# Performance work log

Measured on AMD Instinct MI355X. Metric: run time of the kernel, lower is better.

The kernel has to match this reference:

```python
import jax, jax.numpy as jnp
import numpy as np

B, D, NCOMP, DCOMP = 4096, 2048, 4, 1024  # out_features = NCOMP * DCOMP = 4096


def setup_inputs() -> dict:
    key = jax.random.key(0)
    ks = jax.random.split(key, 6)
    scale = 0.02
    return {
        "x": jax.random.normal(ks[0], (B, D), jnp.float32),
        "noise": jax.random.normal(ks[1], (B, NCOMP), jnp.float32),
        "Wc": jax.random.normal(ks[2], (NCOMP, D, DCOMP), jnp.float32) * scale,
        "bc": jnp.zeros((NCOMP, DCOMP), jnp.float32),
        "Wg": jax.random.normal(ks[3], (D, NCOMP), jnp.float32) * scale,
        "bg": jnp.zeros((NCOMP,), jnp.float32),
        "Wn": jax.random.normal(ks[4], (D, NCOMP), jnp.float32) * scale,
        "bn": jnp.zeros((NCOMP,), jnp.float32),
    }


def reference(x, noise, Wc, bc, Wg, bg, Wn, bn):
    # gating: H = Wg(x) + randn * softplus(Wnoise(x))
    g = x @ Wg + bg                                   # [B, n]
    sp = jax.nn.softplus(x @ Wn + bn)                 # [B, n]
    H = g + noise * sp                                # [B, n]
    # top-1 index, monotonic hard gate: select all components i <= argmax
    k = jnp.argmax(H, axis=1, keepdims=True)          # [B, 1]
    mask = (jnp.arange(H.shape[1])[None, :] <= k).astype(H.dtype)  # [B, n]
    # straight-through: forward value = mask, grad d G/d H = identity
    G = H + jax.lax.stop_gradient(mask - H)
    # all components computed vectorized; unselected ones are zeroed by G
    comps = jnp.einsum('bd,ndo->bno', x, Wc) + bc     # [B, n, DCOMP]
    mask_sg = jax.lax.stop_gradient(mask)
    # multiply by mask_sg so unselected (padded) channels carry no grad path,
    # matching torch which never computes components beyond k (zero pad).
    E = (comps * G[:, :, None] * mask_sg[:, :, None]).reshape(x.shape[0], -1)  # [B, out_features]
    return (E, G)
```

## Files before the change

kernel.cpp:

```cpp
#include <hip/hip_runtime.h>
#include <hip/hip_bf16.h>
#include <math.h>

constexpr int BROWS = 4096;
constexpr int DDIM  = 2048;
constexpr int NCOMP = 4;
constexpr int DCOMP = 1024;
constexpr int NOUT  = NCOMP * DCOMP;

typedef __attribute__((ext_vector_type(8))) short bf16x8;
typedef __attribute__((ext_vector_type(4))) float f32x4;
typedef __attribute__((ext_vector_type(4))) short s16x4;

__device__ __forceinline__ short f2bf(float f) {
  union { float f; unsigned u; } v; v.f = f;
  unsigned r = v.u + 0x7FFFu + ((v.u >> 16) & 1u);
  return (short)(r >> 16);
}

#define GLOAD_LDS16(gptr, lptr) __builtin_amdgcn_global_load_lds( \
    (const __attribute__((address_space(1))) void*)(gptr),        \
    (__attribute__((address_space(3))) void*)(lptr), 16, 0, 0)

__global__ __launch_bounds__(256) void prep_kernel(
    const float* __restrict__ x, const float* __restrict__ noise,
    const float* __restrict__ Wg, const float* __restrict__ bg,
    const float* __restrict__ Wn, const float* __restrict__ bn,
    const float* __restrict__ Wc,
    float* __restrict__ Gout, short* __restrict__ xb, short* __restrict__ WcT) {
  __shared__ float tile[64][65];
  const int bid = blockIdx.x;
  const int tid = threadIdx.x;

  if (bid < 1024) {
    const int lane = tid & 63;
    const int row  = bid * 4 + (tid >> 6);
    const float* xr = x + (size_t)row * DDIM;
    short* xbr = xb + (size_t)row * DDIM;

    float ag[4] = {0.f, 0.f, 0.f, 0.f};
    float an[4] = {0.f, 0.f, 0.f, 0.f};
#pragma unroll
    for (int i = 0; i < 8; i++) {
      int d = i * 256 + lane * 4;
      float4 v = *reinterpret_cast<const float4*>(xr + d);
      s16x4 s; s.x = f2bf(v.x); s.y = f2bf(v.y); s.z = f2bf(v.z); s.w = f2bf(v.w);
      *reinterpret_cast<s16x4*>(xbr + d) = s;
      float xv[4] = {v.x, v.y, v.z, v.w};
#pragma unroll
      for (int j = 0; j < 4; j++) {
        float4 wg = *reinterpret_cast<const float4*>(Wg + 4 * (d + j));
        float4 wn = *reinterpret_cast<const float4*>(Wn + 4 * (d + j));
        ag[0] += xv[j] * wg.x; ag[1] += xv[j] * wg.y;
        ag[2] += xv[j] * wg.z; ag[3] += xv[j] * wg.w;
        an[0] += xv[j] * wn.x; an[1] += xv[j] * wn.y;
        an[2] += xv[j] * wn.z; an[3] += xv[j] * wn.w;
      }
    }
#pragma unroll
    for (int off = 32; off > 0; off >>= 1) {
#pragma unroll
      for (int c = 0; c < 4; c++) {
        ag[c] += __shfl_xor(ag[c], off);
        an[c] += __shfl_xor(an[c], off);
      }
    }
    if (lane == 0) {
      float H[4];
#pragma unroll
      for (int c = 0; c < 4; c++) {
        float v  = an[c] + bn[c];
        float sp = (v > 20.f) ? v : log1pf(expf(v));
        H[c] = (ag[c] + bg[c]) + noise[(size_t)row * NCOMP + c] * sp;
      }
      int k = 0; float best = H[0];
#pragma unroll
      for (int c = 1; c < 4; c++) { if (H[c] > best) { best = H[c]; k = c; } }
#pragma unroll
      for (int c = 0; c < 4; c++)
        Gout[(size_t)row * NCOMP + c] = (c <= k) ? 1.0f : 0.0f;
    }
  } else {
    const int tb  = bid - 1024;
    const int o_t = tb & 15, d_t = (tb >> 4) & 31, c = tb >> 9;
    const int d0 = d_t * 64, o0 = o_t * 64;
    const int col = tid & 63, rb = tid >> 6;

    const float* src = Wc + ((size_t)c * DDIM + d0) * DCOMP + o0;
#pragma unroll
    for (int i = 0; i < 16; i++) {
      int r = rb + i * 4;
      tile[r][col] = src[(size_t)r * DCOMP + col];
    }
    __syncthreads();
    short* dst = WcT + ((size_t)c * DCOMP + o0) * DDIM + d0;
    const int o   = tid >> 2;
    const int dsb = (tid & 3) * 16;
    bf16x8 p0, p1;
#pragma unroll
    for (int k = 0; k < 8; k++) {
      p0[k] = f2bf(tile[dsb + k][o]);
      p1[k] = f2bf(tile[dsb + 8 + k][o]);
    }
    *reinterpret_cast<bf16x8*>(dst + (size_t)o * DDIM + dsb)     = p0;
    *reinterpret_cast<bf16x8*>(dst + (size_t)o * DDIM + dsb + 8) = p1;
  }
}

constexpr int BM = 256, BN = 256, BK = 64;
constexpr int NT = DDIM / BK;
constexpr int HS = 128 * 64;

template<int MB, int NB>
__device__ __forceinline__ void MF(f32x4 (&acc)[8][4], bf16x8 (&a)[4][2], bf16x8 (&b)[2][2]) {
#pragma unroll
  for (int kh = 0; kh < 2; kh++)
#pragma unroll
    for (int ml = 0; ml < 4; ml++)
#pragma unroll
      for (int nl = 0; nl < 2; nl++)
        acc[MB + ml][NB + nl] = __builtin_amdgcn_mfma_f32_16x16x32_bf16(
            a[ml][kh], b[nl][kh], acc[MB + ml][NB + nl], 0, 0, 0);
}

#define PH_TOP(N)                                            \
  asm volatile("s_waitcnt vmcnt(" #N ")" ::: "memory");      \
  __builtin_amdgcn_s_barrier();

#define PH_MFMA(MB, NB, AREG, BREG)                          \
  __builtin_amdgcn_sched_barrier(0);                         \
  __builtin_amdgcn_s_setprio(1);                             \
  MF<MB, NB>(acc, AREG, BREG);                               \
  __builtin_amdgcn_s_setprio(0);

__global__ __launch_bounds__(512, 2) void gemm_kernel(
    const short* __restrict__ xb, const short* __restrict__ wt,
    const float* __restrict__ bc, const float* __restrict__ G,
    float* __restrict__ E) {
  __shared__ short Asm[2][2][HS];
  __shared__ short Bsm[2][2][HS];

  const int tid  = threadIdx.x;
  const int wave = tid >> 6, lane = tid & 63;
  const int wm = wave >> 2, wn = wave & 3;
  const int fr = lane & 15, fq = lane >> 4, l7 = lane & 7;

  const int xcd = blockIdx.x & 7, j = blockIdx.x >> 3;
  const int trow0 = (((xcd >> 1) << 2) + (j & 3)) * BM;
  const int tcol0 = (((xcd & 1) << 3) + (j >> 2)) * BN;

  const short* baseA[2] = { xb + (size_t)(trow0      ) * DDIM,
                            xb + (size_t)(trow0 + 128) * DDIM };
  const short* baseB[2] = { wt + (size_t)(tcol0      ) * DDIM,
                            wt + (size_t)(tcol0 + 128) * DDIM };

  size_t soff[2]; int ldst[2];
#pragma unroll
  for (int l = 0; l < 2; l++) {
    int f = l * 512 + tid;
    int r = f >> 3;
    int s = (f & 7) ^ (r & 7);
    soff[l] = (size_t)r * DDIM + s * 8;
    ldst[l] = (l * 512 + wave * 64) * 8;
  }

  auto STAGE = [&](const short* gb, int t, short* ldsh) {
#pragma unroll
    for (int l = 0; l < 2; l++)
      GLOAD_LDS16(gb + t * 64 + soff[l], ldsh + ldst[l]);
  };
  auto LDA = [&](const short* Ah, bf16x8 (&a)[4][2]) {
#pragma unroll
    for (int ml = 0; ml < 4; ml++) {
      int rh = wm * 64 + ml * 16 + fr;
#pragma unroll
      for (int kh = 0; kh < 2; kh++) {
        int sl = ((kh * 4 + fq) ^ l7) * 8;
        a[ml][kh] = *reinterpret_cast<const bf16x8*>(Ah + rh * 64 + sl);
      }
    }
  };
  auto LDB = [&](const short* Bh, bf16x8 (&b)[2][2]) {
#pragma unroll
    for (int nl = 0; nl < 2; nl++) {
      int ch = wn * 32 + nl * 16 + fr;
#pragma unroll
      for (int kh = 0; kh < 2; kh++) {
        int sl = ((kh * 4 + fq) ^ l7) * 8;
        b[nl][kh] = *reinterpret_cast<const bf16x8*>(Bh + ch * 64 + sl);
      }
    }
  };

  f32x4 acc[8][4];
#pragma unroll
  for (int m = 0; m < 8; m++)
#pragma unroll
    for (int n = 0; n < 4; n++) acc[m][n] = f32x4{0.f, 0.f, 0.f, 0.f};
  bf16x8 aP[4][2], aQ[4][2], bA[2][2], bB[2][2];

  STAGE(baseA[0], 0, &Asm[0][0][0]);
  STAGE(baseB[0], 0, &Bsm[0][0][0]);
  STAGE(baseA[1], 0, &Asm[0][1][0]);
  STAGE(baseB[1], 0, &Bsm[0][1][0]);
  STAGE(baseB[0], 1, &Bsm[1][0][0]);
  STAGE(baseA[1], 1, &Asm[1][1][0]);
  STAGE(baseA[0], 1, &Asm[1][0][0]);
  STAGE(baseB[1], 1, &Bsm[1][1][0]);
  asm volatile("s_waitcnt vmcnt(12)" ::: "memory");
  __builtin_amdgcn_s_barrier();
  LDA(&Asm[0][0][0], aP);
  LDB(&Bsm[0][0][0], bA);

  for (int i = 0; i < NT / 2 - 1; i++) {
    const int t2 = 2 * i + 2, t3 = 2 * i + 3;

    PH_TOP(10);
    LDA(&Asm[0][1][0], aQ);
    STAGE(baseB[0], t2, &Bsm[0][0][0]);
    PH_MFMA(0, 0, aP, bA);
    PH_TOP(10);
    LDB(&Bsm[0][1][0], bB);
    STAGE(baseA[0], t2, &Asm[0][0][0]);
    PH_MFMA(4, 0, aQ, bA);
    PH_TOP(10);
    LDB(&Bsm[1][0][0], bA);
    STAGE(baseA[1], t2, &Asm[0][1][0]);
    PH_MFMA(4, 2, aQ, bB);
    PH_TOP(10);
    LDA(&Asm[1][1][0], aQ);
    STAGE(baseB[1], t2, &Bsm[0][1][0]);
    PH_MFMA(0, 2, aP, bB);
    PH_TOP(10);
    LDA(&Asm[1][0][0], aP);
    STAGE(baseB[0], t3, &Bsm[1][0][0]);
    PH_MFMA(4, 0, aQ, bA);
    PH_TOP(10);
    LDB(&Bsm[1][1][0], bB);
    STAGE(baseA[1], t3, &Asm[1][1][0]);
    PH_MFMA(0, 0, aP, bA);
    PH_TOP(10);
    LDB(&Bsm[0][0][0], bA);
    STAGE(baseA[0], t3, &Asm[1][0][0]);
    PH_MFMA(0, 2, aP, bB);
    PH_TOP(10);
    LDA(&Asm[0][0][0], aP);
    STAGE(baseB[1], t3, &Bsm[1][1][0]);
    PH_MFMA(4, 2, aQ, bB);
  }

  {
    PH_TOP(10);
    LDA(&Asm[0][1][0], aQ);
    PH_MFMA(0, 0, aP, bA);
    PH_TOP(8);
    LDB(&Bsm[0][1][0], bB);
    PH_MFMA(4, 0, aQ, bA);
    PH_TOP(6);
    LDB(&Bsm[1][0][0], bA);
    PH_MFMA(4, 2, aQ, bB);
    PH_TOP(4);
    LDA(&Asm[1][1][0], aQ);
    PH_MFMA(0, 2, aP, bB);
    PH_TOP(2);
    LDA(&Asm[1][0][0], aP);
    PH_MFMA(4, 0, aQ, bA);
    PH_TOP(0);
    LDB(&Bsm[1][1][0], bB);
    PH_MFMA(0, 0, aP, bA);
    __builtin_amdgcn_s_barrier();
    PH_MFMA(0, 2, aP, bB);
    __builtin_amdgcn_s_barrier();
    PH_MFMA(4, 2, aQ, bB);
  }

  const int comp = tcol0 >> 10;
  const float* __restrict__ bcn = bc + (size_t)comp * DCOMP + (tcol0 & (DCOMP - 1));
  float bias[4];
#pragma unroll
  for (int n = 0; n < 4; n++)
    bias[n] = bcn[((n >> 1) * 128) + wn * 32 + (n & 1) * 16 + fr];
#pragma unroll
  for (int m = 0; m < 8; m++) {
    int growb = trow0 + ((m >> 2) * 128) + wm * 64 + (m & 3) * 16 + fq * 4;
#pragma unroll
    for (int j = 0; j < 4; j++) {
      int r = growb + j;
      float mval = G[(size_t)r * NCOMP + comp];
      float* Erow = E + (size_t)r * NOUT + tcol0;
#pragma unroll
      for (int n = 0; n < 4; n++) {
        int coll = ((n >> 1) * 128) + wn * 32 + (n & 1) * 16 + fr;
        Erow[coll] = mval * (acc[m][n][j] + bias[n]);
      }
    }
  }
}

extern "C" void kernel_launch(void* const* d_in, const int* in_sizes, int n_in,
                              void* d_out, int out_size, void* d_ws, size_t ws_size,
                              hipStream_t stream) {
  const float* x     = (const float*)d_in[0];
  const float* noise = (const float*)d_in[1];
  const float* Wc    = (const float*)d_in[2];
  const float* bc    = (const float*)d_in[3];
  const float* Wg    = (const float*)d_in[4];
  const float* bg    = (const float*)d_in[5];
  const float* Wn    = (const float*)d_in[6];
  const float* bn    = (const float*)d_in[7];

  float* E = (float*)d_out;
  float* G = (float*)d_out + (size_t)BROWS * NOUT;

  short* xb  = (short*)d_ws;
  short* WcT = xb + (size_t)BROWS * DDIM;

  prep_kernel<<<3072, 256, 0, stream>>>(x, noise, Wg, bg, Wn, bn, Wc, G, xb, WcT);
  gemm_kernel<<<256, 512, 0, stream>>>(xb, WcT, bc, G, E);
}
```

Measured before the change: 100.4 us.

## Restructure GEMM main loop pipeline with a third A register set and lgkmcnt waits

Reorders the software pipeline of the bf16 MFMA GEMM main loop. It adds a third A-fragment register buffer (aR) and replaces uniform vmcnt-plus-barrier phase tops with finer lgkmcnt/vmcnt waits, and changes the order and timing of global-to-LDS stage issues, including a prologue that stages only seven half-tiles. The aim is to keep LDS reads and global loads in flight across more MFMA phases and cut barrier stalls. It costs extra VGPRs under a 2-blocks-per-CU launch bound, and the hand-tuned wait counts risk races if they are wrong.

```diff
diff --git a/kernel.cpp b/kernel.cpp
--- a/kernel.cpp
+++ b/kernel.cpp
@@ -111,8 +111,13 @@
 constexpr int NT = DDIM / BK;
 constexpr int HS = 128 * 64;
 
+#define WAITLGKM(N) asm volatile("s_waitcnt lgkmcnt(" #N ")" ::: "memory")
+#define WAITVM(N)   asm volatile("s_waitcnt vmcnt(" #N ")" ::: "memory")
+#define BAR         __builtin_amdgcn_s_barrier()
+
 template<int MB, int NB>
 __device__ __forceinline__ void MF(f32x4 (&acc)[8][4], bf16x8 (&a)[4][2], bf16x8 (&b)[2][2]) {
+  __builtin_amdgcn_s_setprio(1);
 #pragma unroll
   for (int kh = 0; kh < 2; kh++)
 #pragma unroll
@@ -121,17 +126,8 @@
       for (int nl = 0; nl < 2; nl++)
         acc[MB + ml][NB + nl] = __builtin_amdgcn_mfma_f32_16x16x32_bf16(
             a[ml][kh], b[nl][kh], acc[MB + ml][NB + nl], 0, 0, 0);
-}
-
-#define PH_TOP(N)                                            \
-  asm volatile("s_waitcnt vmcnt(" #N ")" ::: "memory");      \
-  __builtin_amdgcn_s_barrier();
-
-#define PH_MFMA(MB, NB, AREG, BREG)                          \
-  __builtin_amdgcn_sched_barrier(0);                         \
-  __builtin_amdgcn_s_setprio(1);                             \
-  MF<MB, NB>(acc, AREG, BREG);                               \
   __builtin_amdgcn_s_setprio(0);
+}
 
 __global__ __launch_bounds__(512, 2) void gemm_kernel(
     const short* __restrict__ xb, const short* __restrict__ wt,
@@ -197,81 +193,81 @@
   for (int m = 0; m < 8; m++)
 #pragma unroll
     for (int n = 0; n < 4; n++) acc[m][n] = f32x4{0.f, 0.f, 0.f, 0.f};
-  bf16x8 aP[4][2], aQ[4][2], bA[2][2], bB[2][2];
+  bf16x8 aP[4][2], aQ[4][2], aR[4][2], bA[2][2], bB[2][2];
 
   STAGE(baseA[0], 0, &Asm[0][0][0]);
   STAGE(baseB[0], 0, &Bsm[0][0][0]);
   STAGE(baseA[1], 0, &Asm[0][1][0]);
   STAGE(baseB[1], 0, &Bsm[0][1][0]);
+  STAGE(baseA[0], 1, &Asm[1][0][0]);
   STAGE(baseB[0], 1, &Bsm[1][0][0]);
-  STAGE(baseA[1], 1, &Asm[1][1][0]);
-  STAGE(baseA[0], 1, &Asm[1][0][0]);
   STAGE(baseB[1], 1, &Bsm[1][1][0]);
-  asm volatile("s_waitcnt vmcnt(12)" ::: "memory");
-  __builtin_amdgcn_s_barrier();
+  WAITVM(6);
+  BAR;
   LDA(&Asm[0][0][0], aP);
   LDB(&Bsm[0][0][0], bA);
 
   for (int i = 0; i < NT / 2 - 1; i++) {
-    const int t2 = 2 * i + 2, t3 = 2 * i + 3;
-
-    PH_TOP(10);
+    const int t1 = 2 * i + 1, t2 = 2 * i + 2, t3 = 2 * i + 3;
+
     LDA(&Asm[0][1][0], aQ);
-    STAGE(baseB[0], t2, &Bsm[0][0][0]);
-    PH_MFMA(0, 0, aP, bA);
-    PH_TOP(10);
+    STAGE(baseA[1], t1, &Asm[1][1][0]);
+    WAITLGKM(8); BAR;
+    MF<0, 0>(acc, aP, bA);
     LDB(&Bsm[0][1][0], bB);
     STAGE(baseA[0], t2, &Asm[0][0][0]);
-    PH_MFMA(4, 0, aQ, bA);
-    PH_TOP(10);
-    LDB(&Bsm[1][0][0], bA);
+    WAITLGKM(4); BAR;
+    MF<4, 0>(acc, aQ, bA);
+    WAITLGKM(0); WAITVM(6); BAR;
+    LDA(&Asm[1][0][0], aR); LDB(&Bsm[1][0][0], bA);
+    STAGE(baseB[0], t2, &Bsm[0][0][0]);
+    MF<4, 2>(acc, aQ, bB);
+    STAGE(baseB[1], t2, &Bsm[0][1][0]);
+    BAR;
+    MF<0, 2>(acc, aP, bB);
+    WAITVM(6); BAR;
+    LDA(&Asm[1][1][0], aQ);
     STAGE(baseA[1], t2, &Asm[0][1][0]);
-    PH_MFMA(4, 2, aQ, bB);
-    PH_TOP(10);
+    WAITLGKM(8); BAR;
+    MF<0, 0>(acc, aR, bA);
+    LDB(&Bsm[1][1][0], bB);
+    STAGE(baseA[0], t3, &Asm[1][0][0]);
+    WAITLGKM(4); BAR;
+    MF<4, 0>(acc, aQ, bA);
+    WAITLGKM(0); WAITVM(6); BAR;
+    LDA(&Asm[0][0][0], aP); LDB(&Bsm[0][0][0], bA);
+    STAGE(baseB[0], t3, &Bsm[1][0][0]);
+    MF<4, 2>(acc, aQ, bB);
+    STAGE(baseB[1], t3, &Bsm[1][1][0]);
+    BAR;
+    MF<0, 2>(acc, aR, bB);
+    WAITVM(6); WAITLGKM(0); BAR;
+  }
+
+  {
+    LDA(&Asm[0][1][0], aQ);
+    STAGE(baseA[1], NT - 1, &Asm[1][1][0]);
+    WAITLGKM(8); BAR;
+    MF<0, 0>(acc, aP, bA);
+    LDB(&Bsm[0][1][0], bB);
+    WAITLGKM(4); BAR;
+    MF<4, 0>(acc, aQ, bA);
+    WAITLGKM(0); WAITVM(4); BAR;
+    LDA(&Asm[1][0][0], aR); LDB(&Bsm[1][0][0], bA);
+    MF<4, 2>(acc, aQ, bB);
+    BAR;
+    MF<0, 2>(acc, aP, bB);
+    WAITVM(0); BAR;
     LDA(&Asm[1][1][0], aQ);
-    STAGE(baseB[1], t2, &Bsm[0][1][0]);
-    PH_MFMA(0, 2, aP, bB);
-    PH_TOP(10);
-    LDA(&Asm[1][0][0], aP);
-    STAGE(baseB[0], t3, &Bsm[1][0][0]);
-    PH_MFMA(4, 0, aQ, bA);
-    PH_TOP(10);
+    WAITLGKM(8); BAR;
+    MF<0, 0>(acc, aR, bA);
     LDB(&Bsm[1][1][0], bB);
-    STAGE(baseA[1], t3, &Asm[1][1][0]);
-    PH_MFMA(0, 0, aP, bA);
-    PH_TOP(10);
-    LDB(&Bsm[0][0][0], bA);
-    STAGE(baseA[0], t3, &Asm[1][0][0]);
-    PH_MFMA(0, 2, aP, bB);
-    PH_TOP(10);
-    LDA(&Asm[0][0][0], aP);
-    STAGE(baseB[1], t3, &Bsm[1][1][0]);
-    PH_MFMA(4, 2, aQ, bB);
-  }
-
-  {
-    PH_TOP(10);
-    LDA(&Asm[0][1][0], aQ);
-    PH_MFMA(0, 0, aP, bA);
-    PH_TOP(8);
-    LDB(&Bsm[0][1][0], bB);
-    PH_MFMA(4, 0, aQ, bA);
-    PH_TOP(6);
-    LDB(&Bsm[1][0][0], bA);
-    PH_MFMA(4, 2, aQ, bB);
-    PH_TOP(4);
-    LDA(&Asm[1][1][0], aQ);
-    PH_MFMA(0, 2, aP, bB);
-    PH_TOP(2);
-    LDA(&Asm[1][0][0], aP);
-    PH_MFMA(4, 0, aQ, bA);
-    PH_TOP(0);
-    LDB(&Bsm[1][1][0], bB);
-    PH_MFMA(0, 0, aP, bA);
-    __builtin_amdgcn_s_barrier();
-    PH_MFMA(0, 2, aP, bB);
-    __builtin_amdgcn_s_barrier();
-    PH_MFMA(4, 2, aQ, bB);
+    WAITLGKM(4); BAR;
+    MF<4, 0>(acc, aQ, bA);
+    WAITLGKM(0); BAR;
+    MF<4, 2>(acc, aQ, bB);
+    BAR;
+    MF<0, 2>(acc, aR, bB);
   }
 
   const int comp = tcol0 >> 10;
@@ -284,14 +280,14 @@
   for (int m = 0; m < 8; m++) {
     int growb = trow0 + ((m >> 2) * 128) + wm * 64 + (m & 3) * 16 + fq * 4;
 #pragma unroll
-    for (int j = 0; j < 4; j++) {
-      int r = growb + j;
+    for (int j2 = 0; j2 < 4; j2++) {
+      int r = growb + j2;
       float mval = G[(size_t)r * NCOMP + comp];
       float* Erow = E + (size_t)r * NOUT + tcol0;
 #pragma unroll
       for (int n = 0; n < 4; n++) {
         int coll = ((n >> 1) * 128) + wn * 32 + (n & 1) * 16 + fr;
-        Erow[coll] = mval * (acc[m][n][j] + bias[n]);
+        Erow[coll] = mval * (acc[m][n][j2] + bias[n]);
       }
     }
   }
```

New measurement: 241.3 us. 140% more time.
